# Kernel optimization log

Hardware: AMD Instinct MI355X
Metric: run time of the kernel (lower is better)

## Reference

```python
import jax, jax.numpy as jnp
import numpy as np

B, E, N, D = 2048, 32, 32, 64  # batch, n_entities, n_neighbors, dim


def setup_inputs() -> dict:
    key = jax.random.key(0)
    k1, k2, k3, k4, k5 = jax.random.split(key, 5)
    return {
        "self_vectors": jax.random.normal(k1, (B, E, D), dtype=jnp.float32),
        "neighbor_vectors": jax.random.normal(k2, (B, E, N, D), dtype=jnp.float32),
        "neighbor_relations": jax.random.normal(k3, (B, E, N, D), dtype=jnp.float32),
        "user_embeddings": jax.random.normal(k4, (B, D), dtype=jnp.float32),
        "masks": jnp.ones((B, E), dtype=bool),  # unused by the module
        "W": jax.random.normal(k5, (D, D), dtype=jnp.float32) * (1.0 / np.sqrt(D)),
        "b_lin": jnp.zeros((D,), dtype=jnp.float32),
    }


def reference(self_vectors, neighbor_vectors, neighbor_relations, user_embeddings, masks, W, b_lin):
    # user-relation scores: mean over dim of (user [b,1,1,d] * relations [b,e,n,d])
    scores = jnp.einsum('bd,bend->ben', user_embeddings, neighbor_relations) / neighbor_relations.shape[-1]
    attn = jax.nn.softmax(scores, axis=-1)[..., None]          # [b,e,n,1]
    # torch.mean over neighbor axis of attn * neighbor_vectors
    neighbors_agg = jnp.mean(attn * neighbor_vectors, axis=2)  # [b,e,d]
    out = self_vectors + neighbors_agg                         # [b,e,d]
    out = out @ W.T + b_lin                                    # Linear (dropout p=0 -> identity)
    return jax.nn.relu(out)
```

## Files before the change

### kernel.cpp

```cpp
#include <hip/hip_runtime.h>

#define B_  2048
#define E_  32
#define N_  32
#define D_  64

__global__ __launch_bounds__(256) void kgcn_kernel(
    const float* __restrict__ self_v,
    const float* __restrict__ nv,
    const float* __restrict__ rel,
    const float* __restrict__ user,
    const float* __restrict__ W,
    const float* __restrict__ blin,
    float* __restrict__ out)
{
    const int be = blockIdx.x;
    const int b  = be >> 5;
    const int t  = threadIdx.x;
    const int n0 = t >> 4;
    const int d4 = t & 15;

    __shared__ float  s_score[N_];
    __shared__ float  s_attn[N_];
    __shared__ float4 s_acc[256];
    __shared__ float4 s_pre[D_ / 4];

    const float4* rel4 = (const float4*)rel + (size_t)be * 512;
    const float4* nv4  = (const float4*)nv  + (size_t)be * 512;

    float4 r0 = rel4[t];
    float4 r1 = rel4[t + 256];
    float4 v0 = nv4[t];
    float4 v1 = nv4[t + 256];
    float4 u4 = ((const float4*)user)[b * 16 + d4];

    float p0 = r0.x * u4.x + r0.y * u4.y + r0.z * u4.z + r0.w * u4.w;
    float p1 = r1.x * u4.x + r1.y * u4.y + r1.z * u4.z + r1.w * u4.w;

    #pragma unroll
    for (int m = 1; m < 16; m <<= 1) {
        p0 += __shfl_xor(p0, m);
        p1 += __shfl_xor(p1, m);
    }
    if (d4 == 0) {
        s_score[n0]      = p0 * (1.0f / (float)D_);
        s_score[n0 + 16] = p1 * (1.0f / (float)D_);
    }
    __syncthreads();

    if (t < N_) {
        float m = -1e30f;
        #pragma unroll
        for (int n = 0; n < N_; ++n) m = fmaxf(m, s_score[n]);
        float e = __expf(s_score[t] - m);
        s_attn[t] = e;
    }
    __syncthreads();
    if (t < N_) {
        float s = 0.0f;
        #pragma unroll
        for (int n = 0; n < N_; ++n) s += s_attn[n];
        s_score[t] = s_attn[t] / (s * (float)N_);
    }
    __syncthreads();

    {
        const float a0 = s_score[n0];
        const float a1 = s_score[n0 + 16];
        float4 acc;
        acc.x = a0 * v0.x + a1 * v1.x;
        acc.y = a0 * v0.y + a1 * v1.y;
        acc.z = a0 * v0.z + a1 * v1.z;
        acc.w = a0 * v0.w + a1 * v1.w;
        s_acc[t] = acc;
    }
    __syncthreads();

    if (t < 16) {
        float4 s = s_acc[t];
        #pragma unroll
        for (int k = 1; k < 16; ++k) {
            float4 x = s_acc[t + 16 * k];
            s.x += x.x; s.y += x.y; s.z += x.z; s.w += x.w;
        }
        float4 sv = ((const float4*)self_v)[(size_t)be * 16 + t];
        s.x += sv.x; s.y += sv.y; s.z += sv.z; s.w += sv.w;
        s_pre[t] = s;
    }
    __syncthreads();

    if (t < D_) {
        float acc = blin[t];
        const float4* Wrow = (const float4*)W + t * 16;
        #pragma unroll
        for (int k4 = 0; k4 < 16; ++k4) {
            float4 w = Wrow[k4];
            float4 p = s_pre[k4];
            acc += w.x * p.x + w.y * p.y + w.z * p.z + w.w * p.w;
        }
        out[(size_t)be * 64 + t] = fmaxf(acc, 0.0f);
    }
}

extern "C" void kernel_launch(void* const* d_in, const int* in_sizes, int n_in,
                              void* d_out, int out_size, void* d_ws, size_t ws_size,
                              hipStream_t stream) {
    const float* self_v = (const float*)d_in[0];
    const float* nv     = (const float*)d_in[1];
    const float* rel    = (const float*)d_in[2];
    const float* user   = (const float*)d_in[3];
    const float* W      = (const float*)d_in[5];
    const float* blin   = (const float*)d_in[6];
    float* out          = (float*)d_out;

    const int blocks = B_ * E_;
    kgcn_kernel<<<blocks, 256, 0, stream>>>(self_v, nv, rel, user, W, blin, out);
}
```

Baseline: 1.009 ms.

## Assign one wavefront per (batch, entity) and replace block syncs with shuffles

Each 64-lane wave now handles one (b,e) row instead of a 256-thread block, so four rows share a block. Score reduction, softmax and neighbor aggregation run in registers with cross-lane shuffles instead of shared memory and __syncthreads, and the final linear layer is done by all 64 lanes. Streaming loads and stores use nontemporal hints. This cuts barrier and idle-thread overhead in a memory-bound kernel, at the cost of more registers per thread (16 float4 values live at once).

```diff
diff --git a/kernel.cpp b/kernel.cpp
--- a/kernel.cpp
+++ b/kernel.cpp
@@ -5,7 +5,11 @@
 #define N_  32
 #define D_  64
 
-__global__ __launch_bounds__(256) void kgcn_kernel(
+typedef float f4 __attribute__((ext_vector_type(4)));
+
+__device__ __forceinline__ float shflx(float v, int m) { return __shfl_xor(v, m, 64); }
+
+__global__ __launch_bounds__(256) void kgcn_wave(
     const float* __restrict__ self_v,
     const float* __restrict__ nv,
     const float* __restrict__ rel,
@@ -14,92 +18,77 @@
     const float* __restrict__ blin,
     float* __restrict__ out)
 {
-    const int be = blockIdx.x;
+    const int t  = threadIdx.x;
+    const int w  = t >> 6;
+    const int l  = t & 63;
+    const int g  = l >> 4;
+    const int d4 = l & 15;
+
+    const int be = blockIdx.x * 4 + w;
     const int b  = be >> 5;
-    const int t  = threadIdx.x;
-    const int n0 = t >> 4;
-    const int d4 = t & 15;
 
-    __shared__ float  s_score[N_];
-    __shared__ float  s_attn[N_];
-    __shared__ float4 s_acc[256];
-    __shared__ float4 s_pre[D_ / 4];
+    __shared__ f4 s_pre[4][16];
 
-    const float4* rel4 = (const float4*)rel + (size_t)be * 512;
-    const float4* nv4  = (const float4*)nv  + (size_t)be * 512;
+    const f4* rel4 = (const f4*)rel + (size_t)be * 512;
+    const f4* nv4  = (const f4*)nv  + (size_t)be * 512;
 
-    float4 r0 = rel4[t];
-    float4 r1 = rel4[t + 256];
-    float4 v0 = nv4[t];
-    float4 v1 = nv4[t + 256];
-    float4 u4 = ((const float4*)user)[b * 16 + d4];
+    f4 u4 = ((const f4*)user)[b * 16 + d4];
+    f4 r[8], v[8];
+    #pragma unroll
+    for (int j = 0; j < 8; ++j) r[j] = __builtin_nontemporal_load(&rel4[j * 64 + l]);
+    #pragma unroll
+    for (int j = 0; j < 8; ++j) v[j] = __builtin_nontemporal_load(&nv4[j * 64 + l]);
+    f4 sv = ((const f4*)self_v)[(size_t)be * 16 + d4];
 
-    float p0 = r0.x * u4.x + r0.y * u4.y + r0.z * u4.z + r0.w * u4.w;
-    float p1 = r1.x * u4.x + r1.y * u4.y + r1.z * u4.z + r1.w * u4.w;
+    float s[8];
+    #pragma unroll
+    for (int j = 0; j < 8; ++j) {
+        float p = r[j].x * u4.x + r[j].y * u4.y + r[j].z * u4.z + r[j].w * u4.w;
+        p += shflx(p, 1); p += shflx(p, 2); p += shflx(p, 4); p += shflx(p, 8);
+        s[j] = p * (1.0f / (float)D_);
+    }
 
+    float m = s[0];
     #pragma unroll
-    for (int m = 1; m < 16; m <<= 1) {
-        p0 += __shfl_xor(p0, m);
-        p1 += __shfl_xor(p1, m);
+    for (int j = 1; j < 8; ++j) m = fmaxf(m, s[j]);
+    m = fmaxf(m, shflx(m, 16));
+    m = fmaxf(m, shflx(m, 32));
+
+    float e[8];
+    float sum = 0.0f;
+    #pragma unroll
+    for (int j = 0; j < 8; ++j) { e[j] = __expf(s[j] - m); sum += e[j]; }
+    sum += shflx(sum, 16);
+    sum += shflx(sum, 32);
+    const float sc = 1.0f / (sum * (float)N_);
+
+    f4 acc = (f4){0.0f, 0.0f, 0.0f, 0.0f};
+    #pragma unroll
+    for (int j = 0; j < 8; ++j) {
+        const float a = e[j] * sc;
+        acc.x += a * v[j].x;
+        acc.y += a * v[j].y;
+        acc.z += a * v[j].z;
+        acc.w += a * v[j].w;
     }
-    if (d4 == 0) {
-        s_score[n0]      = p0 * (1.0f / (float)D_);
-        s_score[n0 + 16] = p1 * (1.0f / (float)D_);
+    acc.x += shflx(acc.x, 16); acc.y += shflx(acc.y, 16);
+    acc.z += shflx(acc.z, 16); acc.w += shflx(acc.w, 16);
+    acc.x += shflx(acc.x, 32); acc.y += shflx(acc.y, 32);
+    acc.z += shflx(acc.z, 32); acc.w += shflx(acc.w, 32);
+
+    acc.x += sv.x; acc.y += sv.y; acc.z += sv.z; acc.w += sv.w;
+    if (g == 0) s_pre[w][d4] = acc;
+    __builtin_amdgcn_wave_barrier();
+
+    float o = blin[l];
+    const f4* Wrow = (const f4*)W + l * 16;
+    #pragma unroll
+    for (int k4 = 0; k4 < 16; ++k4) {
+        f4 wv = Wrow[k4];
+        f4 p  = s_pre[w][k4];
+        o += wv.x * p.x + wv.y * p.y + wv.z * p.z + wv.w * p.w;
     }
-    __syncthreads();
-
-    if (t < N_) {
-        float m = -1e30f;
-        #pragma unroll
-        for (int n = 0; n < N_; ++n) m = fmaxf(m, s_score[n]);
-        float e = __expf(s_score[t] - m);
-        s_attn[t] = e;
-    }
-    __syncthreads();
-    if (t < N_) {
-        float s = 0.0f;
-        #pragma unroll
-        for (int n = 0; n < N_; ++n) s += s_attn[n];
-        s_score[t] = s_attn[t] / (s * (float)N_);
-    }
-    __syncthreads();
-
-    {
-        const float a0 = s_score[n0];
-        const float a1 = s_score[n0 + 16];
-        float4 acc;
-        acc.x = a0 * v0.x + a1 * v1.x;
-        acc.y = a0 * v0.y + a1 * v1.y;
-        acc.z = a0 * v0.z + a1 * v1.z;
-        acc.w = a0 * v0.w + a1 * v1.w;
-        s_acc[t] = acc;
-    }
-    __syncthreads();
-
-    if (t < 16) {
-        float4 s = s_acc[t];
-        #pragma unroll
-        for (int k = 1; k < 16; ++k) {
-            float4 x = s_acc[t + 16 * k];
-            s.x += x.x; s.y += x.y; s.z += x.z; s.w += x.w;
-        }
-        float4 sv = ((const float4*)self_v)[(size_t)be * 16 + t];
-        s.x += sv.x; s.y += sv.y; s.z += sv.z; s.w += sv.w;
-        s_pre[t] = s;
-    }
-    __syncthreads();
-
-    if (t < D_) {
-        float acc = blin[t];
-        const float4* Wrow = (const float4*)W + t * 16;
-        #pragma unroll
-        for (int k4 = 0; k4 < 16; ++k4) {
-            float4 w = Wrow[k4];
-            float4 p = s_pre[k4];
-            acc += w.x * p.x + w.y * p.y + w.z * p.z + w.w * p.w;
-        }
-        out[(size_t)be * 64 + t] = fmaxf(acc, 0.0f);
-    }
+    __builtin_nontemporal_store(fmaxf(o, 0.0f), &out[(size_t)be * 64 + l]);
 }
 
 extern "C" void kernel_launch(void* const* d_in, const int* in_sizes, int n_in,
@@ -113,6 +102,6 @@
     const float* blin   = (const float*)d_in[6];
     float* out          = (float*)d_out;
 
-    const int blocks = B_ * E_;
-    kgcn_kernel<<<blocks, 256, 0, stream>>>(self_v, nv, rel, user, W, blin, out);
+    const int blocks = (B_ * E_) / 4;
+    kgcn_wave<<<blocks, 256, 0, stream>>>(self_v, nv, rel, user, W, blin, out);
 }
```

Result: no change. 1.008 ms (-0.1%).
